# Performance work log

Hardware: AMD Instinct MI355X
Metric: run time of the kernel (lower is better)

The kernel has to match this reference:

```python
import jax, jax.numpy as jnp
import numpy as np

N, S, D_IN, ATTN_DIM, OUT_DIM = 4, 8192, 1024, 1024, 1024


def setup_inputs() -> dict:
    key = jax.random.key(0)
    ks = jax.random.split(key, 6)
    scale_in = 1.0 / np.sqrt(D_IN)
    scale_attn = 1.0 / np.sqrt(ATTN_DIM)
    return {
        "x": jax.random.normal(ks[0], (N, S, D_IN), dtype=jnp.float32),
        "wq": jax.random.normal(ks[1], (D_IN, ATTN_DIM), dtype=jnp.float32) * scale_in,
        "bq": jnp.zeros((ATTN_DIM,), dtype=jnp.float32),
        "wk": jax.random.normal(ks[2], (D_IN, ATTN_DIM), dtype=jnp.float32) * scale_in,
        "bk": jnp.zeros((ATTN_DIM,), dtype=jnp.float32),
        "wv": jax.random.normal(ks[3], (D_IN, ATTN_DIM), dtype=jnp.float32) * scale_in,
        "bv": jnp.zeros((ATTN_DIM,), dtype=jnp.float32),
        "wo": jax.random.normal(ks[4], (ATTN_DIM, OUT_DIM), dtype=jnp.float32) * scale_attn,
        "bo": jnp.zeros((OUT_DIM,), dtype=jnp.float32),
    }


def reference(x, wq, bq, wk, bk, wv, bv, wo, bo):
    # QKV projections (Dense layers)
    query = x @ wq + bq  # [n, s, h]
    key_ = x @ wk + bk
    value = x @ wv + bv
    # elu+1 feature map
    Q = jax.nn.elu(query) + 1.0
    K = jax.nn.elu(key_) + 1.0
    # per-channel global reductions over sequence (einsum 'nsh,nsh->nh')
    KV = jnp.einsum('nsh,nsh->nh', K, value, precision='highest')  # [n, h]
    Ksum = jnp.sum(K, axis=1)  # [n, h]
    Z = 1.0 / (Q * Ksum[:, None, :] + 1e-6)  # [n, s, h]
    V = Q * KV[:, None, :] * Z  # [n, s, h]
    out = V @ wo + bo
    return jax.nn.gelu(out, approximate=True)
```

## Files before the change

### kernel.cpp

```cpp
#include <hip/hip_runtime.h>
#include <math.h>
#include <stdint.h>


#define S_LEN 8192

typedef __attribute__((ext_vector_type(8))) __bf16 bf16x8;
typedef __attribute__((ext_vector_type(8))) unsigned short ushort8;
typedef __attribute__((ext_vector_type(4))) float f32x4;

__device__ __forceinline__ unsigned short f2bf(float f) {
    unsigned int u = __builtin_bit_cast(unsigned int, f);
    unsigned int r = (u + 0x7fffu + ((u >> 16) & 1u)) >> 16;
    return (unsigned short)r;
}
__device__ __forceinline__ float bf2f(unsigned short s) {
    unsigned int u = ((unsigned int)s) << 16;
    return __builtin_bit_cast(float, u);
}
__device__ __forceinline__ float elu1(float v) { return v > 0.f ? v + 1.f : __expf(v); }
__device__ __forceinline__ float gelu_tanh(float v) {
    float u = 1.5957691216057308f * (v + 0.044715f * v * v * v);
    float e = __expf(u);
    float th = 1.f - 2.f / (e + 1.f);
    return 0.5f * v * (1.f + th);
}
__device__ __forceinline__ void glds16(const void* g, void* l) {
    __builtin_amdgcn_global_load_lds(
        (const __attribute__((address_space(1))) unsigned int*)(uintptr_t)g,
        (__attribute__((address_space(3))) unsigned int*)(uintptr_t)l, 16, 0, 0);
}

#define KBAR()  asm volatile("s_barrier" ::: "memory")
#define VM4()   asm volatile("s_waitcnt vmcnt(4)" ::: "memory")
#define VM0()   asm volatile("s_waitcnt vmcnt(0)" ::: "memory")

#define LDF(P, OFF) __builtin_bit_cast(bf16x8, *(const ushort8*)&(P)[OFF])

__global__ __launch_bounds__(256) void xconv(const float* __restrict__ x,
                                             unsigned short* __restrict__ xb)
{
    const size_t base = ((size_t)blockIdx.x * 256 + threadIdx.x) * 8;
    float4 a = *(const float4*)&x[base];
    float4 b = *(const float4*)&x[base + 4];
    ushort8 o;
    o[0] = f2bf(a.x); o[1] = f2bf(a.y); o[2] = f2bf(a.z); o[3] = f2bf(a.w);
    o[4] = f2bf(b.x); o[5] = f2bf(b.y); o[6] = f2bf(b.z); o[7] = f2bf(b.w);
    *(ushort8*)&xb[base] = o;
}

__global__ __launch_bounds__(256) void wtrans(const float* __restrict__ wq,
                                              const float* __restrict__ wk,
                                              const float* __restrict__ wv,
                                              const float* __restrict__ wo,
                                              unsigned short* __restrict__ wT)
{
    __shared__ float tile[64][65];
    const int z = blockIdx.z;
    const float* w = (z == 0) ? wq : (z == 1) ? wk : (z == 2) ? wv : wo;
    unsigned short* dst = wT + (size_t)z * 1048576;
    const int t  = threadIdx.x;
    const int n0 = blockIdx.x * 64;
    const int k0 = blockIdx.y * 64;
    const int r  = t >> 2;
    const int c4 = (t & 3) * 16;
    #pragma unroll
    for (int j = 0; j < 4; ++j) {
        float4 v = *(const float4*)&w[(size_t)(k0 + r) * 1024 + n0 + c4 + j * 4];
        tile[r][c4 + j * 4 + 0] = v.x; tile[r][c4 + j * 4 + 1] = v.y;
        tile[r][c4 + j * 4 + 2] = v.z; tile[r][c4 + j * 4 + 3] = v.w;
    }
    __syncthreads();
    const int nn = t >> 2;
    const int kc = (t & 3) * 16;
    ushort8 o0, o1;
    #pragma unroll
    for (int j = 0; j < 8; ++j) o0[j] = f2bf(tile[kc + j][nn]);
    #pragma unroll
    for (int j = 0; j < 8; ++j) o1[j] = f2bf(tile[kc + 8 + j][nn]);
    *(ushort8*)&dst[(size_t)(n0 + nn) * 1024 + k0 + kc]     = o0;
    *(ushort8*)&dst[(size_t)(n0 + nn) * 1024 + k0 + kc + 8] = o1;
}

__global__ __launch_bounds__(512) void qkv_mfma(
    const unsigned short* __restrict__ xb,
    const unsigned short* __restrict__ wqT,
    const unsigned short* __restrict__ wkT,
    const unsigned short* __restrict__ wvT,
    const float* __restrict__ bq, const float* __restrict__ bk,
    const float* __restrict__ bv,
    unsigned short* __restrict__ Qout,
    float* __restrict__ KV, float* __restrict__ Ks,
    int moff)
{
    __shared__ unsigned short Alds[3][256 * 64];
    __shared__ unsigned short Blds[2][3][64 * 64];
    __shared__ float redkv[16][64];
    __shared__ float redks[16][64];

    const int t = threadIdx.x;
    const unsigned int nlin = blockIdx.x + 16u * blockIdx.y;
    const unsigned int swz  = (nlin & 7u) * 128u + (nlin >> 3);
    const int h0   = (int)(swz & 15u) * 64;
    const int m0   = (int)(swz >> 4) * 256;
    const int mg   = moff + m0;
    const int bidx = mg >> 13;

    const int lane = t & 63, wid = t >> 6;
    const int wm = wid >> 1, wn = wid & 1;
    const int lr = lane & 15, quad = lane >> 4;

    const int sA   = wid * 64 + lane;
    const int xks0 = ((quad)     ^ (lr & 7)) * 8;
    const int xks1 = ((quad | 4) ^ (lr & 7)) * 8;
    const int arow = (wm * 64 + lr) * 64;
    const int brow = (wn * 32 + lr) * 64;

    auto stA = [&](int kt, int u, int buf) {
        const int s = u * 512 + sA;
        const int r = s >> 3;
        const int j = (s & 7) ^ (r & 7);
        glds16(&xb[(size_t)(m0 + r) * 1024 + kt * 64 + j * 8],
               &Alds[buf][(u * 512 + wid * 64) * 8]);
    };
    auto stB = [&](const unsigned short* w, int mat, int kt, int buf) {
        const int r = sA >> 3;
        const int j = (sA & 7) ^ (r & 7);
        glds16(&w[(size_t)(h0 + r) * 1024 + kt * 64 + j * 8],
               &Blds[buf][mat][wid * 512]);
    };

    f32x4 accq[4][2], acck[4][2], accv[4][2];
    #pragma unroll
    for (int mi = 0; mi < 4; ++mi)
        #pragma unroll
        for (int nj = 0; nj < 2; ++nj) {
            accq[mi][nj] = (f32x4){0.f, 0.f, 0.f, 0.f};
            acck[mi][nj] = (f32x4){0.f, 0.f, 0.f, 0.f};
            accv[mi][nj] = (f32x4){0.f, 0.f, 0.f, 0.f};
        }

    #pragma unroll
    for (int u = 0; u < 4; ++u) stA(0, u, 0);
    stB(wqT, 0, 0, 0); stB(wkT, 1, 0, 0); stB(wvT, 2, 0, 0);
    #pragma unroll
    for (int u = 0; u < 4; ++u) stA(1, u, 1);
    VM4();
    KBAR();

    #pragma unroll
    for (int kt = 0; kt < 16; ++kt) {
        const int ab = kt % 3;
        const int bb = kt & 1;
        bf16x8 af0[4], af1[4], b0[3][2], b1[3][2];
        #pragma unroll
        for (int mi = 0; mi < 4; ++mi)
            af0[mi] = LDF(Alds[ab], arow + mi * 1024 + xks0);
        #pragma unroll
        for (int mt = 0; mt < 3; ++mt)
            #pragma unroll
            for (int nj = 0; nj < 2; ++nj)
                b0[mt][nj] = LDF(Blds[bb][mt], brow + nj * 1024 + xks0);
        if (kt + 1 < 16) {
            stB(wqT, 0, kt + 1, (kt + 1) & 1);
            stB(wkT, 1, kt + 1, (kt + 1) & 1);
            stB(wvT, 2, kt + 1, (kt + 1) & 1);
        }
        if (kt + 2 < 16) {
            stA(kt + 2, 0, (kt + 2) % 3); stA(kt + 2, 1, (kt + 2) % 3);
            stA(kt + 2, 2, (kt + 2) % 3); stA(kt + 2, 3, (kt + 2) % 3);
        }
        #pragma unroll
        for (int mi = 0; mi < 4; ++mi)
            af1[mi] = LDF(Alds[ab], arow + mi * 1024 + xks1);
        #pragma unroll
        for (int mt = 0; mt < 3; ++mt)
            #pragma unroll
            for (int nj = 0; nj < 2; ++nj)
                b1[mt][nj] = LDF(Blds[bb][mt], brow + nj * 1024 + xks1);

        __builtin_amdgcn_s_setprio(1);
        #pragma unroll
        for (int mi = 0; mi < 4; ++mi)
            #pragma unroll
            for (int nj = 0; nj < 2; ++nj) {
                accq[mi][nj] = __builtin_amdgcn_mfma_f32_16x16x32_bf16(af0[mi], b0[0][nj], accq[mi][nj], 0, 0, 0);
                acck[mi][nj] = __builtin_amdgcn_mfma_f32_16x16x32_bf16(af0[mi], b0[1][nj], acck[mi][nj], 0, 0, 0);
                accv[mi][nj] = __builtin_amdgcn_mfma_f32_16x16x32_bf16(af0[mi], b0[2][nj], accv[mi][nj], 0, 0, 0);
            }
        #pragma unroll
        for (int mi = 0; mi < 4; ++mi)
            #pragma unroll
            for (int nj = 0; nj < 2; ++nj) {
                accq[mi][nj] = __builtin_amdgcn_mfma_f32_16x16x32_bf16(af1[mi], b1[0][nj], accq[mi][nj], 0, 0, 0);
                acck[mi][nj] = __builtin_amdgcn_mfma_f32_16x16x32_bf16(af1[mi], b1[1][nj], acck[mi][nj], 0, 0, 0);
                accv[mi][nj] = __builtin_amdgcn_mfma_f32_16x16x32_bf16(af1[mi], b1[2][nj], accv[mi][nj], 0, 0, 0);
            }
        __builtin_amdgcn_s_setprio(0);

        if (kt <= 13)      VM4();
        else if (kt == 14) VM0();
        if (kt < 15) KBAR();
    }

    float bqv[2], bkv[2], bvv[2];
    #pragma unroll
    for (int nj = 0; nj < 2; ++nj) {
        const int h = h0 + wn * 32 + nj * 16 + lr;
        bqv[nj] = bq[h]; bkv[nj] = bk[h]; bvv[nj] = bv[h];
    }
    float kvp[2] = {0.f, 0.f}, ksp[2] = {0.f, 0.f};
    #pragma unroll
    for (int mi = 0; mi < 4; ++mi)
        #pragma unroll
        for (int nj = 0; nj < 2; ++nj) {
            const int h = h0 + wn * 32 + nj * 16 + lr;
            #pragma unroll
            for (int r = 0; r < 4; ++r) {
                const int m = mg + wm * 64 + mi * 16 + quad * 4 + r;
                float q = elu1(accq[mi][nj][r] + bqv[nj]);
                Qout[(size_t)m * 1024 + h] = f2bf(q);
                float kk = elu1(acck[mi][nj][r] + bkv[nj]);
                float vv = accv[mi][nj][r] + bvv[nj];
                kvp[nj] = fmaf(kk, vv, kvp[nj]);
                ksp[nj] += kk;
            }
        }
    #pragma unroll
    for (int nj = 0; nj < 2; ++nj) {
        redkv[wm * 4 + quad][wn * 32 + nj * 16 + lr] = kvp[nj];
        redks[wm * 4 + quad][wn * 32 + nj * 16 + lr] = ksp[nj];
    }
    __syncthreads();
    if (t < 64) {
        float s = 0.f;
        #pragma unroll
        for (int g = 0; g < 16; ++g) s += redkv[g][t];
        atomicAdd(&KV[bidx * 1024 + h0 + t], s);
    } else if (t < 128) {
        const int c = t - 64;
        float s = 0.f;
        #pragma unroll
        for (int g = 0; g < 16; ++g) s += redks[g][c];
        atomicAdd(&Ks[bidx * 1024 + h0 + c], s);
    }
}

__global__ __launch_bounds__(256) void vprime(
    unsigned short* __restrict__ Q,
    const float* __restrict__ KV, const float* __restrict__ Ks)
{
    const size_t idx  = (size_t)blockIdx.x * 256 + threadIdx.x;
    const size_t base = idx * 8;
    const int h = (int)(base & 1023);
    const int n = (int)(base >> 23);
    ushort8 q8 = *(ushort8*)&Q[base];
    const float* kvp = &KV[n * 1024 + h];
    const float* ksp = &Ks[n * 1024 + h];
    ushort8 o;
    #pragma unroll
    for (int j = 0; j < 8; ++j) {
        float qf = bf2f(q8[j]);
        float vp = qf * kvp[j] * __builtin_amdgcn_rcpf(fmaf(qf, ksp[j], 1e-6f));
        o[j] = f2bf(vp);
    }
    *(ushort8*)&Q[base] = o;
}

__global__ __launch_bounds__(512) void out_mfma(
    const unsigned short* __restrict__ Vp,
    const unsigned short* __restrict__ woT,
    const float* __restrict__ bo, float* __restrict__ out)
{
    __shared__ unsigned short Alds[3][256 * 64];
    __shared__ unsigned short Blds[2][256 * 64];

    const int t  = threadIdx.x;
    const unsigned int nlin = blockIdx.x + 4u * blockIdx.y;
    const unsigned int swz  = (nlin & 7u) * 64u + (nlin >> 3);
    const int h0 = (int)(swz & 3u) * 256;
    const int m0 = (int)(swz >> 2) * 256;

    const int lane = t & 63, wid = t >> 6;
    const int wm = wid >> 2, wn = wid & 3;
    const int lr = lane & 15, quad = lane >> 4;

    const int sA   = wid * 64 + lane;
    const int xks0 = ((quad)     ^ (lr & 7)) * 8;
    const int xks1 = ((quad | 4) ^ (lr & 7)) * 8;
    const int arow = (wm * 128 + lr) * 64;
    const int brow = (wn * 64 + lr) * 64;

    auto stA = [&](int kt, int u, int buf) {
        const int s = u * 512 + sA;
        const int r = s >> 3;
        const int j = (s & 7) ^ (r & 7);
        glds16(&Vp[(size_t)(m0 + r) * 1024 + kt * 64 + j * 8],
               &Alds[buf][(u * 512 + wid * 64) * 8]);
    };
    auto stB = [&](int kt, int u, int buf) {
        const int s = u * 512 + sA;
        const int r = s >> 3;
        const int j = (s & 7) ^ (r & 7);
        glds16(&woT[(size_t)(h0 + r) * 1024 + kt * 64 + j * 8],
               &Blds[buf][(u * 512 + wid * 64) * 8]);
    };

    f32x4 acc[8][4];
    #pragma unroll
    for (int mr = 0; mr < 8; ++mr)
        #pragma unroll
        for (int nc = 0; nc < 4; ++nc) acc[mr][nc] = (f32x4){0.f, 0.f, 0.f, 0.f};

    #pragma unroll
    for (int u = 0; u < 4; ++u) stA(0, u, 0);
    #pragma unroll
    for (int u = 0; u < 4; ++u) stB(0, u, 0);
    #pragma unroll
    for (int u = 0; u < 4; ++u) stA(1, u, 1);
    VM4();
    KBAR();

    #pragma unroll
    for (int kt = 0; kt < 16; ++kt) {
        const int ab = kt % 3;
        const int bb = kt & 1;
        bf16x8 af[2][8], bfr[2][4];
        #pragma unroll
        for (int mh = 0; mh < 2; ++mh)
            #pragma unroll
            for (int mi = 0; mi < 4; ++mi)
                af[0][mh * 4 + mi] = LDF(Alds[ab], arow + mh * 4096 + mi * 1024 + xks0);
        #pragma unroll
        for (int nh = 0; nh < 2; ++nh)
            #pragma unroll
            for (int nj = 0; nj < 2; ++nj)
                bfr[0][nh * 2 + nj] = LDF(Blds[bb], brow + nh * 2048 + nj * 1024 + xks0);
        if (kt + 1 < 16) {
            stB(kt + 1, 0, (kt + 1) & 1); stB(kt + 1, 1, (kt + 1) & 1);
            stB(kt + 1, 2, (kt + 1) & 1); stB(kt + 1, 3, (kt + 1) & 1);
        }
        if (kt + 2 < 16) {
            stA(kt + 2, 0, (kt + 2) % 3); stA(kt + 2, 1, (kt + 2) % 3);
            stA(kt + 2, 2, (kt + 2) % 3); stA(kt + 2, 3, (kt + 2) % 3);
        }
        #pragma unroll
        for (int mh = 0; mh < 2; ++mh)
            #pragma unroll
            for (int mi = 0; mi < 4; ++mi)
                af[1][mh * 4 + mi] = LDF(Alds[ab], arow + mh * 4096 + mi * 1024 + xks1);
        #pragma unroll
        for (int nh = 0; nh < 2; ++nh)
            #pragma unroll
            for (int nj = 0; nj < 2; ++nj)
                bfr[1][nh * 2 + nj] = LDF(Blds[bb], brow + nh * 2048 + nj * 1024 + xks1);

        __builtin_amdgcn_s_setprio(1);
        #pragma unroll
        for (int s = 0; s < 2; ++s)
            #pragma unroll
            for (int mr = 0; mr < 8; ++mr)
                #pragma unroll
                for (int nc = 0; nc < 4; ++nc)
                    acc[mr][nc] = __builtin_amdgcn_mfma_f32_16x16x32_bf16(
                        af[s][mr], bfr[s][nc], acc[mr][nc], 0, 0, 0);
        __builtin_amdgcn_s_setprio(0);

        if (kt <= 13)      VM4();
        else if (kt == 14) VM0();
        if (kt < 15) KBAR();
    }

    float bov[4];
    #pragma unroll
    for (int nc = 0; nc < 4; ++nc) bov[nc] = bo[h0 + wn * 64 + nc * 16 + lr];
    #pragma unroll
    for (int mr = 0; mr < 8; ++mr)
        #pragma unroll
        for (int nc = 0; nc < 4; ++nc) {
            const int h = h0 + wn * 64 + nc * 16 + lr;
            #pragma unroll
            for (int r = 0; r < 4; ++r) {
                const int m = m0 + wm * 128 + mr * 16 + quad * 4 + r;
                out[(size_t)m * 1024 + h] = gelu_tanh(acc[mr][nc][r] + bov[nc]);
            }
        }
}

extern "C" void kernel_launch(void* const* d_in, const int* in_sizes, int n_in,
                              void* d_out, int out_size, void* d_ws, size_t ws_size,
                              hipStream_t stream)
{
    const float* x  = (const float*)d_in[0];
    const float* wq = (const float*)d_in[1];
    const float* bq = (const float*)d_in[2];
    const float* wk = (const float*)d_in[3];
    const float* bk = (const float*)d_in[4];
    const float* wv = (const float*)d_in[5];
    const float* bv = (const float*)d_in[6];
    const float* wo = (const float*)d_in[7];
    const float* bo = (const float*)d_in[8];
    float* out = (float*)d_out;

    char* wsb = (char*)d_ws;
    unsigned short* Qws = (unsigned short*)wsb;
    unsigned short* xb  = (unsigned short*)(wsb + 67108864ULL);
    unsigned short* wqT = (unsigned short*)(wsb + 100663296ULL);
    unsigned short* wkT = wqT + 1048576;
    unsigned short* wvT = wkT + 1048576;
    unsigned short* woT = wvT + 1048576;
    float* KV = (float*)(wsb + 100663296ULL + 4ULL * 2097152);
    float* Ks = KV + 4 * 1024;

    hipMemsetAsync(KV, 0, 2 * 4 * 1024 * sizeof(float), stream);

    wtrans<<<dim3(16, 16, 4), 256, 0, stream>>>(wq, wk, wv, wo, wqT);

    for (int half = 0; half < 2; ++half) {
        xconv<<<8192, 256, 0, stream>>>(x + (size_t)half * 16384 * 1024, xb);
        qkv_mfma<<<dim3(16, 64), 512, 0, stream>>>(xb, wqT, wkT, wvT, bq, bk, bv,
                                                   Qws, KV, Ks, half * 16384);
    }
    vprime<<<16384, 256, 0, stream>>>(Qws, KV, Ks);
    out_mfma<<<dim3(4, 128), 512, 0, stream>>>(Qws, woT, bo, out);
}
```

Before: 517.0 us.

## Restructure GEMM pipelines to double-buffered LDS with register prefetch and 2 blocks/CU

Result: faster. 498.9 us (-3.5%).

```diff
diff --git a/kernel.cpp b/kernel.cpp
--- a/kernel.cpp
+++ b/kernel.cpp
@@ -32,7 +32,10 @@
 }
 
 #define KBAR()  asm volatile("s_barrier" ::: "memory")
-#define VM4()   asm volatile("s_waitcnt vmcnt(4)" ::: "memory")
+#define LGKM0() do { asm volatile("s_waitcnt lgkmcnt(0)" ::: "memory"); \
+                     __builtin_amdgcn_sched_barrier(0); } while (0)
+#define VM8()   asm volatile("s_waitcnt vmcnt(8)" ::: "memory")
+#define VM7()   asm volatile("s_waitcnt vmcnt(7)" ::: "memory")
 #define VM0()   asm volatile("s_waitcnt vmcnt(0)" ::: "memory")
 
 #define LDF(P, OFF) __builtin_bit_cast(bf16x8, *(const ushort8*)&(P)[OFF])
@@ -82,7 +85,7 @@
     *(ushort8*)&dst[(size_t)(n0 + nn) * 1024 + k0 + kc + 8] = o1;
 }
 
-__global__ __launch_bounds__(512) void qkv_mfma(
+__global__ __launch_bounds__(512, 2) void qkv_mfma(
     const unsigned short* __restrict__ xb,
     const unsigned short* __restrict__ wqT,
     const unsigned short* __restrict__ wkT,
@@ -93,7 +96,7 @@
     float* __restrict__ KV, float* __restrict__ Ks,
     int moff)
 {
-    __shared__ unsigned short Alds[3][256 * 64];
+    __shared__ unsigned short Alds[2][256 * 64];
     __shared__ unsigned short Blds[2][3][64 * 64];
     __shared__ float redkv[16][64];
     __shared__ float redks[16][64];
@@ -145,31 +148,23 @@
     stB(wqT, 0, 0, 0); stB(wkT, 1, 0, 0); stB(wvT, 2, 0, 0);
     #pragma unroll
     for (int u = 0; u < 4; ++u) stA(1, u, 1);
-    VM4();
+    stB(wqT, 0, 1, 1); stB(wkT, 1, 1, 1); stB(wvT, 2, 1, 1);
+    VM7();
     KBAR();
 
+    bf16x8 af0[4], af1[4], b0[3][2], b1[3][2];
+    #pragma unroll
+    for (int mi = 0; mi < 4; ++mi)
+        af0[mi] = LDF(Alds[0], arow + mi * 1024 + xks0);
+    #pragma unroll
+    for (int mt = 0; mt < 3; ++mt)
+        #pragma unroll
+        for (int nj = 0; nj < 2; ++nj)
+            b0[mt][nj] = LDF(Blds[0][mt], brow + nj * 1024 + xks0);
+
     #pragma unroll
     for (int kt = 0; kt < 16; ++kt) {
-        const int ab = kt % 3;
-        const int bb = kt & 1;
-        bf16x8 af0[4], af1[4], b0[3][2], b1[3][2];
-        #pragma unroll
-        for (int mi = 0; mi < 4; ++mi)
-            af0[mi] = LDF(Alds[ab], arow + mi * 1024 + xks0);
-        #pragma unroll
-        for (int mt = 0; mt < 3; ++mt)
-            #pragma unroll
-            for (int nj = 0; nj < 2; ++nj)
-                b0[mt][nj] = LDF(Blds[bb][mt], brow + nj * 1024 + xks0);
-        if (kt + 1 < 16) {
-            stB(wqT, 0, kt + 1, (kt + 1) & 1);
-            stB(wkT, 1, kt + 1, (kt + 1) & 1);
-            stB(wvT, 2, kt + 1, (kt + 1) & 1);
-        }
-        if (kt + 2 < 16) {
-            stA(kt + 2, 0, (kt + 2) % 3); stA(kt + 2, 1, (kt + 2) % 3);
-            stA(kt + 2, 2, (kt + 2) % 3); stA(kt + 2, 3, (kt + 2) % 3);
-        }
+        const int ab = kt & 1, nb = (kt + 1) & 1;
         #pragma unroll
         for (int mi = 0; mi < 4; ++mi)
             af1[mi] = LDF(Alds[ab], arow + mi * 1024 + xks1);
@@ -177,8 +172,7 @@
         for (int mt = 0; mt < 3; ++mt)
             #pragma unroll
             for (int nj = 0; nj < 2; ++nj)
-                b1[mt][nj] = LDF(Blds[bb][mt], brow + nj * 1024 + xks1);
-
+                b1[mt][nj] = LDF(Blds[ab][mt], brow + nj * 1024 + xks1);
         __builtin_amdgcn_s_setprio(1);
         #pragma unroll
         for (int mi = 0; mi < 4; ++mi)
@@ -188,6 +182,29 @@
                 acck[mi][nj] = __builtin_amdgcn_mfma_f32_16x16x32_bf16(af0[mi], b0[1][nj], acck[mi][nj], 0, 0, 0);
                 accv[mi][nj] = __builtin_amdgcn_mfma_f32_16x16x32_bf16(af0[mi], b0[2][nj], accv[mi][nj], 0, 0, 0);
             }
+        __builtin_amdgcn_s_setprio(0);
+
+        if (kt < 15) {
+            VM0();
+            LGKM0();
+            KBAR();
+            #pragma unroll
+            for (int mi = 0; mi < 4; ++mi)
+                af0[mi] = LDF(Alds[nb], arow + mi * 1024 + xks0);
+            #pragma unroll
+            for (int mt = 0; mt < 3; ++mt)
+                #pragma unroll
+                for (int nj = 0; nj < 2; ++nj)
+                    b0[mt][nj] = LDF(Blds[nb][mt], brow + nj * 1024 + xks0);
+            if (kt + 2 < 16) {
+                stB(wqT, 0, kt + 2, ab);
+                stB(wkT, 1, kt + 2, ab);
+                stB(wvT, 2, kt + 2, ab);
+                stA(kt + 2, 0, ab); stA(kt + 2, 1, ab);
+                stA(kt + 2, 2, ab); stA(kt + 2, 3, ab);
+            }
+        }
+        __builtin_amdgcn_s_setprio(1);
         #pragma unroll
         for (int mi = 0; mi < 4; ++mi)
             #pragma unroll
@@ -197,10 +214,6 @@
                 accv[mi][nj] = __builtin_amdgcn_mfma_f32_16x16x32_bf16(af1[mi], b1[2][nj], accv[mi][nj], 0, 0, 0);
             }
         __builtin_amdgcn_s_setprio(0);
-
-        if (kt <= 13)      VM4();
-        else if (kt == 14) VM0();
-        if (kt < 15) KBAR();
     }
 
     float bqv[2], bkv[2], bvv[2];
@@ -267,12 +280,12 @@
     *(ushort8*)&Q[base] = o;
 }
 
-__global__ __launch_bounds__(512) void out_mfma(
+__global__ __launch_bounds__(512, 2) void out_mfma(
     const unsigned short* __restrict__ Vp,
     const unsigned short* __restrict__ woT,
     const float* __restrict__ bo, float* __restrict__ out)
 {
-    __shared__ unsigned short Alds[3][256 * 64];
+    __shared__ unsigned short Alds[2][256 * 64];
     __shared__ unsigned short Blds[2][256 * 64];
 
     const int t  = threadIdx.x;
@@ -318,57 +331,74 @@
     for (int u = 0; u < 4; ++u) stB(0, u, 0);
     #pragma unroll
     for (int u = 0; u < 4; ++u) stA(1, u, 1);
-    VM4();
+    #pragma unroll
+    for (int u = 0; u < 4; ++u) stB(1, u, 1);
+    VM8();
     KBAR();
 
+    bf16x8 af0[8], af1[8], b0[4], b1[4];
+    #pragma unroll
+    for (int mh = 0; mh < 2; ++mh)
+        #pragma unroll
+        for (int mi = 0; mi < 4; ++mi)
+            af0[mh * 4 + mi] = LDF(Alds[0], arow + mh * 4096 + mi * 1024 + xks0);
+    #pragma unroll
+    for (int nh = 0; nh < 2; ++nh)
+        #pragma unroll
+        for (int nj = 0; nj < 2; ++nj)
+            b0[nh * 2 + nj] = LDF(Blds[0], brow + nh * 2048 + nj * 1024 + xks0);
+
     #pragma unroll
     for (int kt = 0; kt < 16; ++kt) {
-        const int ab = kt % 3;
-        const int bb = kt & 1;
-        bf16x8 af[2][8], bfr[2][4];
+        const int ab = kt & 1, nb = (kt + 1) & 1;
         #pragma unroll
         for (int mh = 0; mh < 2; ++mh)
             #pragma unroll
             for (int mi = 0; mi < 4; ++mi)
-                af[0][mh * 4 + mi] = LDF(Alds[ab], arow + mh * 4096 + mi * 1024 + xks0);
+                af1[mh * 4 + mi] = LDF(Alds[ab], arow + mh * 4096 + mi * 1024 + xks1);
         #pragma unroll
         for (int nh = 0; nh < 2; ++nh)
             #pragma unroll
             for (int nj = 0; nj < 2; ++nj)
-                bfr[0][nh * 2 + nj] = LDF(Blds[bb], brow + nh * 2048 + nj * 1024 + xks0);
-        if (kt + 1 < 16) {
-            stB(kt + 1, 0, (kt + 1) & 1); stB(kt + 1, 1, (kt + 1) & 1);
-            stB(kt + 1, 2, (kt + 1) & 1); stB(kt + 1, 3, (kt + 1) & 1);
+                b1[nh * 2 + nj] = LDF(Blds[ab], brow + nh * 2048 + nj * 1024 + xks1);
+        __builtin_amdgcn_s_setprio(1);
+        #pragma unroll
+        for (int mr = 0; mr < 8; ++mr)
+            #pragma unroll
+            for (int nc = 0; nc < 4; ++nc)
+                acc[mr][nc] = __builtin_amdgcn_mfma_f32_16x16x32_bf16(
+                    af0[mr], b0[nc], acc[mr][nc], 0, 0, 0);
+        __builtin_amdgcn_s_setprio(0);
+
+        if (kt < 15) {
+            VM0();
+            LGKM0();
+            KBAR();
+            #pragma unroll
+            for (int mh = 0; mh < 2; ++mh)
+                #pragma unroll
+                for (int mi = 0; mi < 4; ++mi)
+                    af0[mh * 4 + mi] = LDF(Alds[nb], arow + mh * 4096 + mi * 1024 + xks0);
+            #pragma unroll
+            for (int nh = 0; nh < 2; ++nh)
+                #pragma unroll
+                for (int nj = 0; nj < 2; ++nj)
+                    b0[nh * 2 + nj] = LDF(Blds[nb], brow + nh * 2048 + nj * 1024 + xks0);
+            if (kt + 2 < 16) {
+                stB(kt + 2, 0, ab); stB(kt + 2, 1, ab);
+                stB(kt + 2, 2, ab); stB(kt + 2, 3, ab);
+                stA(kt + 2, 0, ab); stA(kt + 2, 1, ab);
+                stA(kt + 2, 2, ab); stA(kt + 2, 3, ab);
+            }
         }
-        if (kt + 2 < 16) {
-            stA(kt + 2, 0, (kt + 2) % 3); stA(kt + 2, 1, (kt + 2) % 3);
-            stA(kt + 2, 2, (kt + 2) % 3); stA(kt + 2, 3, (kt + 2) % 3);
-        }
-        #pragma unroll
-        for (int mh = 0; mh < 2; ++mh)
-            #pragma unroll
-            for (int mi = 0; mi < 4; ++mi)
-                af[1][mh * 4 + mi] = LDF(Alds[ab], arow + mh * 4096 + mi * 1024 + xks1);
-        #pragma unroll
-        for (int nh = 0; nh < 2; ++nh)
-            #pragma unroll
-            for (int nj = 0; nj < 2; ++nj)
-                bfr[1][nh * 2 + nj] = LDF(Blds[bb], brow + nh * 2048 + nj * 1024 + xks1);
-
         __builtin_amdgcn_s_setprio(1);
         #pragma unroll
-        for (int s = 0; s < 2; ++s)
-            #pragma unroll
-            for (int mr = 0; mr < 8; ++mr)
-                #pragma unroll
-                for (int nc = 0; nc < 4; ++nc)
-                    acc[mr][nc] = __builtin_amdgcn_mfma_f32_16x16x32_bf16(
-                        af[s][mr], bfr[s][nc], acc[mr][nc], 0, 0, 0);
+        for (int mr = 0; mr < 8; ++mr)
+            #pragma unroll
+            for (int nc = 0; nc < 4; ++nc)
+                acc[mr][nc] = __builtin_amdgcn_mfma_f32_16x16x32_bf16(
+                    af1[mr], b1[nc], acc[mr][nc], 0, 0, 0);
         __builtin_amdgcn_s_setprio(0);
-
-        if (kt <= 13)      VM4();
-        else if (kt == 14) VM0();
-        if (kt < 15) KBAR();
     }
 
     float bov[4];
```
